# Kernel optimization log

Hardware: AMD Instinct MI355X
Metric: run time of the kernel (lower is better)

The kernel has to match this reference:

```python
import jax, jax.numpy as jnp
import numpy as np

VOCAB = 32000
D_MODEL = 1024
HIDDEN = 2 * D_MODEL
NUM_EXPERTS = 8
TOP_K = 2
B, S = 2, 1024
LN_EPS = 1e-5


def setup_inputs() -> dict:
    key = jax.random.key(0)
    ks = jax.random.split(key, 12)
    sc = 0.02
    return {
        "x": jax.random.randint(ks[0], (B, S), 0, VOCAB),
        "embed": jax.random.normal(ks[1], (VOCAB, D_MODEL), jnp.float32) * sc,
        "Wg": jax.random.normal(ks[2], (D_MODEL, NUM_EXPERTS), jnp.float32) * sc,
        "bg": jnp.zeros((NUM_EXPERTS,), jnp.float32),
        "W1": jax.random.normal(ks[3], (NUM_EXPERTS, D_MODEL, HIDDEN), jnp.float32) * sc,
        "b1": jnp.zeros((NUM_EXPERTS, HIDDEN), jnp.float32),
        "W2": jax.random.normal(ks[4], (NUM_EXPERTS, HIDDEN, D_MODEL), jnp.float32) * sc,
        "b2": jnp.zeros((NUM_EXPERTS, D_MODEL), jnp.float32),
        "gamma": jnp.ones((D_MODEL,), jnp.float32),
        "beta": jnp.zeros((D_MODEL,), jnp.float32),
        "Wh": jax.random.normal(ks[5], (D_MODEL, VOCAB), jnp.float32) * sc,
        "bh": jnp.zeros((VOCAB,), jnp.float32),
    }


def reference(x, embed, Wg, bg, W1, b1, W2, b2, gamma, beta, Wh, bh):
    # forward_pre: embed + gate softmax + top-k
    h = embed[x]                                     # [B,S,d]
    probs = jax.nn.softmax(h @ Wg + bg, axis=-1)     # [B,S,E]
    topk_vals, topk_idx = jax.lax.top_k(probs, TOP_K)  # [B,S,K]
    # combine weights scattered back to dense expert axis: [B,S,E]
    w = jnp.sum(jax.nn.one_hot(topk_idx, NUM_EXPERTS, dtype=h.dtype)
                * topk_vals[..., None], axis=-2)
    # per-expert FFN run densely, masked-combined by gate weights
    a = jax.nn.relu(jnp.einsum('bsd,edh->bseh', h, W1) + b1)   # [B,S,E,H]
    y = jnp.einsum('bseh,ehd->bsed', a, W2) + b2               # [B,S,E,d]
    combined = jnp.einsum('bsed,bse->bsd', y, w)               # [B,S,d]
    # forward_post: LayerNorm + head
    mu = jnp.mean(combined, axis=-1, keepdims=True)
    var = jnp.var(combined, axis=-1, keepdims=True)
    out = (combined - mu) * jax.lax.rsqrt(var + LN_EPS) * gamma + beta
    logits = out @ Wh + bh                                     # [B,S,V]
    return logits.reshape(-1, VOCAB)
```

## Files before the change

kernel.cpp:

```cpp
#include <hip/hip_runtime.h>
#include <hip/hip_bf16.h>
#include <stdint.h>

#define TOKENS 2048
#define DMODEL 1024
#define HID    2048
#define NEXP   8
#define VOCAB  32000
#define ROWCAP 5120
#define MAXTILES 40
#define LN_EPS 1e-5f

typedef __hip_bfloat16 bf16;
typedef __bf16 v8bf __attribute__((ext_vector_type(8)));
typedef float  v4f  __attribute__((ext_vector_type(4)));

#define CTL_COUNTS 0
#define CTL_CURSOR 8
#define CTL_PADOFF 16
#define CTL_TILE2E 32
#define CTL_NTILES 72
#define CTL_INTS   80

typedef __attribute__((address_space(3))) uint32_t lds_u32_t;
typedef __attribute__((address_space(1))) uint32_t glb_u32_t;

__device__ __forceinline__ void gl2lds16(const void* g, void* l) {
  __builtin_amdgcn_global_load_lds((glb_u32_t*)(uintptr_t)g,
                                   (lds_u32_t*)(uintptr_t)l, 16, 0, 0);
}

__global__ __launch_bounds__(256) void embed_gate(
    const int* __restrict__ x, const float* __restrict__ embed,
    const float* __restrict__ Wg, const float* __restrict__ bg,
    bf16* __restrict__ h_bf, int* __restrict__ top2i, float* __restrict__ top2w,
    int* __restrict__ ctl)
{
  const int t = blockIdx.x, tid = threadIdx.x;
  const int xid = x[t];
  const float4 hv = ((const float4*)(embed + (size_t)xid * DMODEL))[tid];

  union { ushort4 u; bf16 b[4]; } pk;
  pk.b[0] = __float2bfloat16(hv.x); pk.b[1] = __float2bfloat16(hv.y);
  pk.b[2] = __float2bfloat16(hv.z); pk.b[3] = __float2bfloat16(hv.w);
  ((ushort4*)(h_bf + (size_t)t * DMODEL))[tid] = pk.u;

  float acc[8] = {0,0,0,0,0,0,0,0};
  const float hk[4] = {hv.x, hv.y, hv.z, hv.w};
  #pragma unroll
  for (int u = 0; u < 4; ++u) {
    const float* wr = Wg + (size_t)(tid*4 + u) * NEXP;
    #pragma unroll
    for (int e = 0; e < 8; ++e) acc[e] += hk[u] * wr[e];
  }
  #pragma unroll
  for (int e = 0; e < 8; ++e)
    for (int off = 32; off >= 1; off >>= 1)
      acc[e] += __shfl_down(acc[e], off, 64);

  __shared__ float sred[4][8];
  const int lane = tid & 63, wave = tid >> 6;
  if (lane == 0) {
    #pragma unroll
    for (int e = 0; e < 8; ++e) sred[wave][e] = acc[e];
  }
  __syncthreads();
  if (tid == 0) {
    float lg[8];
    #pragma unroll
    for (int e = 0; e < 8; ++e)
      lg[e] = sred[0][e] + sred[1][e] + sred[2][e] + sred[3][e] + bg[e];
    float m = lg[0];
    #pragma unroll
    for (int e = 1; e < 8; ++e) m = fmaxf(m, lg[e]);
    float p[8], s = 0.f;
    #pragma unroll
    for (int e = 0; e < 8; ++e) { p[e] = expf(lg[e] - m); s += p[e]; }
    const float inv = 1.f / s;
    int i0 = 0;
    for (int e = 1; e < 8; ++e) if (p[e] > p[i0]) i0 = e;
    int i1 = -1;
    for (int e = 0; e < 8; ++e) { if (e == i0) continue; if (i1 < 0 || p[e] > p[i1]) i1 = e; }
    top2i[2*t] = i0; top2i[2*t+1] = i1;
    top2w[2*t] = p[i0]*inv; top2w[2*t+1] = p[i1]*inv;
    atomicAdd(&ctl[CTL_COUNTS + i0], 1);
    atomicAdd(&ctl[CTL_COUNTS + i1], 1);
  }
}

__global__ __launch_bounds__(256) void scatter_k(
    const int* __restrict__ top2i, int* __restrict__ ctl,
    int* __restrict__ tok2row, int* __restrict__ rowtok)
{
  __shared__ int spad[8];
  const int tid = threadIdx.x;
  for (int r = tid; r < ROWCAP; r += 256) rowtok[r] = 0;
  if (tid == 0) {
    int off = 0, gm = 0;
    for (int e = 0; e < 8; ++e) {
      spad[e] = off; ctl[CTL_PADOFF + e] = off;
      int nt = (ctl[CTL_COUNTS + e] + 127) >> 7;
      for (int i = 0; i < nt; ++i) ctl[CTL_TILE2E + gm++] = e;
      off += nt << 7;
    }
    ctl[CTL_PADOFF + 8] = off;
    ctl[CTL_NTILES] = gm;
  }
  __syncthreads();
  for (int idx = tid; idx < 2*TOKENS; idx += 256) {
    const int e = top2i[idx];
    const int pos = spad[e] + atomicAdd(&ctl[CTL_CURSOR + e], 1);
    tok2row[idx] = pos;
    rowtok[pos] = idx >> 1;
  }
}

__global__ __launch_bounds__(256) void transpose_cvt(
    const float* __restrict__ in, bf16* __restrict__ out, int R, int C)
{
  __shared__ float tile[32][33];
  const int b = blockIdx.z;
  in  += (size_t)b * R * C;
  out += (size_t)b * R * C;
  const int ct = blockIdx.x * 32, rt = blockIdx.y * 32;
  const int lc = threadIdx.x & 31, lr = threadIdx.x >> 5;
  #pragma unroll
  for (int i = 0; i < 4; ++i) {
    const int r = lr + i*8;
    tile[r][lc] = in[(size_t)(rt + r) * C + ct + lc];
  }
  __syncthreads();
  #pragma unroll
  for (int i = 0; i < 4; ++i) {
    const int r = lr + i*8;
    out[(size_t)(ct + r) * R + rt + lc] = __float2bfloat16(tile[lc][r]);
  }
}

template<int MODE>
__global__ __launch_bounds__(256) void gemm128(
    const bf16* __restrict__ Abase, const bf16* __restrict__ Btbase,
    const float* __restrict__ bias, float* __restrict__ outF, bf16* __restrict__ outB,
    const int* __restrict__ ctl, const int* __restrict__ rowtok)
{
  constexpr int K = (MODE == 1) ? HID : DMODEL;
  constexpr int N = (MODE == 0) ? HID : ((MODE == 1) ? DMODEL : VOCAB);
  const int gm = blockIdx.x, gn = blockIdx.y;

  int eid = 0;
  if constexpr (MODE == 0 || MODE == 1) {
    if (gm >= ctl[CTL_NTILES]) return;
    eid = ctl[CTL_TILE2E + gm];
  }

  __shared__ bf16 As[128 * 32];
  __shared__ bf16 Bs[128 * 32];
  __shared__ int  rts[128];

  const int tid = threadIdx.x, lane = tid & 63, wave = tid >> 6;
  const bf16* Bt = Btbase + (size_t)eid * (size_t)N * K + (size_t)(gn * 128) * K;
  const float* bv = bias + (size_t)eid * N + gn * 128;

  if constexpr (MODE == 0) {
    if (tid < 128) rts[tid] = rowtok[gm * 128 + tid];
    __syncthreads();
  }

  const int srow = lane >> 2;
  const int scol = (lane & 3) * 8;
  const int r0 = wave * 16 + srow, r1 = (wave + 4) * 16 + srow;
  size_t ga0, ga1;
  if constexpr (MODE == 0) { ga0 = (size_t)rts[r0]; ga1 = (size_t)rts[r1]; }
  else { ga0 = (size_t)(gm * 128 + r0); ga1 = (size_t)(gm * 128 + r1); }
  const bf16* aptr0 = Abase + ga0 * K + scol;
  const bf16* aptr1 = Abase + ga1 * K + scol;
  const bf16* bptr0 = Bt + (size_t)r0 * K + scol;
  const bf16* bptr1 = Bt + (size_t)r1 * K + scol;

  const int wm = (wave & 1) * 64, wn = (wave >> 1) * 64;
  const int lr = lane & 15, lq = lane >> 4;

  v4f acc[4][4] = {};

  for (int k0 = 0; k0 < K; k0 += 32) {
    gl2lds16(aptr0 + k0, &As[wave * 512]);
    gl2lds16(aptr1 + k0, &As[(wave + 4) * 512]);
    gl2lds16(bptr0 + k0, &Bs[wave * 512]);
    gl2lds16(bptr1 + k0, &Bs[(wave + 4) * 512]);
    __syncthreads();

    v8bf af[4], bfg[4];
    #pragma unroll
    for (int i = 0; i < 4; ++i) af[i]  = *(const v8bf*)&As[(wm + i*16 + lr) * 32 + lq * 8];
    #pragma unroll
    for (int j = 0; j < 4; ++j) bfg[j] = *(const v8bf*)&Bs[(wn + j*16 + lr) * 32 + lq * 8];
    #pragma unroll
    for (int i = 0; i < 4; ++i)
      #pragma unroll
      for (int j = 0; j < 4; ++j)
        acc[i][j] = __builtin_amdgcn_mfma_f32_16x16x32_bf16(af[i], bfg[j], acc[i][j], 0, 0, 0);
    __syncthreads();
  }

  float bb[4];
  #pragma unroll
  for (int j = 0; j < 4; ++j) bb[j] = bv[wn + j*16 + lr];

  #pragma unroll
  for (int i = 0; i < 4; ++i) {
    #pragma unroll
    for (int j = 0; j < 4; ++j) {
      #pragma unroll
      for (int r = 0; r < 4; ++r) {
        const int row = gm * 128 + wm + i*16 + lq*4 + r;
        const int col = gn * 128 + wn + j*16 + lr;
        float v = acc[i][j][r] + bb[j];
        if constexpr (MODE == 0) {
          v = v > 0.f ? v : 0.f;
          outB[(size_t)row * N + col] = __float2bfloat16(v);
        } else {
          outF[(size_t)row * (size_t)N + col] = v;
        }
      }
    }
  }
}

__global__ __launch_bounds__(256) void combine_ln(
    const float* __restrict__ y, const int* __restrict__ tok2row,
    const float* __restrict__ top2w, const float* __restrict__ gamma,
    const float* __restrict__ beta, bf16* __restrict__ ln)
{
  const int t = blockIdx.x, tid = threadIdx.x;
  const int rr0 = tok2row[2*t], rr1 = tok2row[2*t+1];
  const float w0 = top2w[2*t], w1 = top2w[2*t+1];
  const float4 a = ((const float4*)(y + (size_t)rr0 * DMODEL))[tid];
  const float4 b = ((const float4*)(y + (size_t)rr1 * DMODEL))[tid];
  const float c0 = w0*a.x + w1*b.x, c1 = w0*a.y + w1*b.y;
  const float c2 = w0*a.z + w1*b.z, c3 = w0*a.w + w1*b.w;

  float s1 = c0 + c1 + c2 + c3;
  float s2 = c0*c0 + c1*c1 + c2*c2 + c3*c3;
  for (int off = 32; off >= 1; off >>= 1) {
    s1 += __shfl_down(s1, off, 64);
    s2 += __shfl_down(s2, off, 64);
  }
  __shared__ float rs1[4], rs2[4];
  __shared__ float smu, srs;
  const int lane = tid & 63, wave = tid >> 6;
  if (lane == 0) { rs1[wave] = s1; rs2[wave] = s2; }
  __syncthreads();
  if (tid == 0) {
    const float S1 = rs1[0] + rs1[1] + rs1[2] + rs1[3];
    const float S2 = rs2[0] + rs2[1] + rs2[2] + rs2[3];
    const float mu = S1 / DMODEL;
    const float var = S2 / DMODEL - mu * mu;
    smu = mu; srs = rsqrtf(var + LN_EPS);
  }
  __syncthreads();
  const float mu = smu, rstd = srs;
  const float4 g  = ((const float4*)gamma)[tid];
  const float4 be = ((const float4*)beta)[tid];
  union { ushort4 u; bf16 bb[4]; } pk;
  pk.bb[0] = __float2bfloat16((c0 - mu) * rstd * g.x + be.x);
  pk.bb[1] = __float2bfloat16((c1 - mu) * rstd * g.y + be.y);
  pk.bb[2] = __float2bfloat16((c2 - mu) * rstd * g.z + be.z);
  pk.bb[3] = __float2bfloat16((c3 - mu) * rstd * g.w + be.w);
  ((ushort4*)(ln + (size_t)t * DMODEL))[tid] = pk.u;
}

extern "C" void kernel_launch(void* const* d_in, const int* in_sizes, int n_in,
                              void* d_out, int out_size, void* d_ws, size_t ws_size,
                              hipStream_t stream)
{
  (void)in_sizes; (void)n_in; (void)out_size; (void)ws_size;
  const int*   x     = (const int*)d_in[0];
  const float* embed = (const float*)d_in[1];
  const float* Wg    = (const float*)d_in[2];
  const float* bg    = (const float*)d_in[3];
  const float* W1    = (const float*)d_in[4];
  const float* b1    = (const float*)d_in[5];
  const float* W2    = (const float*)d_in[6];
  const float* b2    = (const float*)d_in[7];
  const float* gamma = (const float*)d_in[8];
  const float* beta  = (const float*)d_in[9];
  const float* Wh    = (const float*)d_in[10];
  const float* bh    = (const float*)d_in[11];
  float* out = (float*)d_out;

  char* ws = (char*)d_ws;
  size_t o = 0;
  int* ctl = (int*)(ws + o);        o += 1024;
  bf16* h_bf = (bf16*)(ws + o);     o += (size_t)TOKENS * DMODEL * 2;
  int* top2i = (int*)(ws + o);      o += (size_t)TOKENS * 2 * 4;
  float* top2w = (float*)(ws + o);  o += (size_t)TOKENS * 2 * 4;
  int* tok2row = (int*)(ws + o);    o += (size_t)TOKENS * 2 * 4;
  int* rowtok = (int*)(ws + o);     o += (size_t)ROWCAP * 4;
  o = (o + 255) & ~(size_t)255;
  bf16* a_act = (bf16*)(ws + o);    o += (size_t)ROWCAP * HID * 2;
  float* yrow = (float*)(ws + o);   o += (size_t)ROWCAP * DMODEL * 4;
  bf16* lnb = (bf16*)(ws + o);      o += (size_t)TOKENS * DMODEL * 2;
  bf16* W1t = (bf16*)(ws + o);      o += (size_t)NEXP * DMODEL * HID * 2;
  bf16* W2t = (bf16*)(ws + o);      o += (size_t)NEXP * DMODEL * HID * 2;
  bf16* Wht = (bf16*)(ws + o);      o += (size_t)DMODEL * VOCAB * 2;

  hipMemsetAsync(ctl, 0, CTL_INTS * sizeof(int), stream);
  embed_gate<<<TOKENS, 256, 0, stream>>>(x, embed, Wg, bg, h_bf, top2i, top2w, ctl);
  scatter_k<<<1, 256, 0, stream>>>(top2i, ctl, tok2row, rowtok);
  transpose_cvt<<<dim3(HID/32, DMODEL/32, NEXP), 256, 0, stream>>>(W1, W1t, DMODEL, HID);
  transpose_cvt<<<dim3(DMODEL/32, HID/32, NEXP), 256, 0, stream>>>(W2, W2t, HID, DMODEL);
  transpose_cvt<<<dim3(VOCAB/32, DMODEL/32, 1), 256, 0, stream>>>(Wh, Wht, DMODEL, VOCAB);
  gemm128<0><<<dim3(MAXTILES, HID/128), 256, 0, stream>>>(h_bf, W1t, b1, nullptr, a_act, ctl, rowtok);
  gemm128<1><<<dim3(MAXTILES, DMODEL/128), 256, 0, stream>>>(a_act, W2t, b2, yrow, nullptr, ctl, nullptr);
  combine_ln<<<TOKENS, 256, 0, stream>>>(yrow, tok2row, top2w, gamma, beta, lnb);
  gemm128<2><<<dim3(TOKENS/128, VOCAB/128), 256, 0, stream>>>(lnb, Wht, bh, out, nullptr, nullptr, nullptr);
}
```

Baseline: 866.8 us.

## Replace head GEMM with 256x256-tile, 512-thread double-buffered MFMA kernel

Replaces the vocab-projection GEMM, previously a 128x128-tile kernel, with a dedicated 256x256-tile kernel. It uses 8 waves, 128KB of dynamic LDS with double buffering via direct global-to-LDS loads, interleaved stage/compute phases with priority hints and sched barriers, and a remapped block order for L2 locality. The head GEMM dominates runtime, and larger tiles cut global and LDS traffic per FLOP while overlapping loads with MFMA work. The risks are lower occupancy from the large LDS footprint and correctness that depends on hand-counted vmcnt waits.

```diff
diff --git a/kernel.cpp b/kernel.cpp
--- a/kernel.cpp
+++ b/kernel.cpp
@@ -144,14 +144,12 @@
     const int* __restrict__ ctl, const int* __restrict__ rowtok)
 {
   constexpr int K = (MODE == 1) ? HID : DMODEL;
-  constexpr int N = (MODE == 0) ? HID : ((MODE == 1) ? DMODEL : VOCAB);
+  constexpr int N = (MODE == 0) ? HID : DMODEL;
   const int gm = blockIdx.x, gn = blockIdx.y;
 
   int eid = 0;
-  if constexpr (MODE == 0 || MODE == 1) {
-    if (gm >= ctl[CTL_NTILES]) return;
-    eid = ctl[CTL_TILE2E + gm];
-  }
+  if (gm >= ctl[CTL_NTILES]) return;
+  eid = ctl[CTL_TILE2E + gm];
 
   __shared__ bf16 As[128 * 32];
   __shared__ bf16 Bs[128 * 32];
@@ -224,6 +222,161 @@
       }
     }
   }
+}
+
+
+__device__ __forceinline__ void stageAB(const bf16* g, char* l) {
+  gl2lds16(g,      l);
+  gl2lds16(g + 32, l + 8192);
+}
+
+#define SBAR() do { __builtin_amdgcn_sched_barrier(0); \
+                    __builtin_amdgcn_s_barrier();       \
+                    __builtin_amdgcn_sched_barrier(0); } while (0)
+
+__global__ __launch_bounds__(512, 2) void gemm256(
+    const bf16* __restrict__ A, const bf16* __restrict__ Bt,
+    const float* __restrict__ bias, float* __restrict__ out)
+{
+  extern __shared__ char smem[];
+  constexpr int K = DMODEL;
+  constexpr int N = VOCAB;
+  constexpr int NK = K / 64;
+
+  const int orig = blockIdx.y * 8 + blockIdx.x;
+  const int p = (orig & 7) * 125 + (orig >> 3);
+  const int tm0 = (p & 7) * 256;
+  const int tn0 = (p >> 3) * 256;
+
+  const int tid = threadIdx.x;
+  const int lane = tid & 63, wv = tid >> 6;
+  const int lr = lane & 15, lq = lane >> 4;
+  const int wr = wv >> 2, wc = wv & 3;
+
+  const int r_s = tid >> 2;
+  const int c_s = (tid & 3) * 8;
+  const bf16* aG = A  + (size_t)(tm0 + r_s) * K + c_s;
+  const bf16* bG = Bt + (size_t)(tn0 + r_s) * K + c_s;
+  char* lW = smem + wv * 1024;
+
+  const int aOff = wr * 16384 + lr * 64 + lq * 16;
+  const int bOff = 32768 + (wc >> 1) * 16384 + ((wc & 1) * 64 + lr) * 64 + lq * 16;
+
+  v4f acc[8][4] = {};
+  v8bf Af[4][2], Bf[4][2];
+
+  stageAB(aG,          lW);
+  stageAB(aG + 131072, lW + 16384);
+  stageAB(bG,          lW + 32768);
+  stageAB(bG + 131072, lW + 32768 + 16384);
+  stageAB(aG + 64,           lW + 65536);
+  stageAB(aG + 131072 + 64,  lW + 65536 + 16384);
+  stageAB(bG + 64,           lW + 65536 + 32768);
+  stageAB(bG + 131072 + 64,  lW + 65536 + 32768 + 16384);
+  asm volatile("s_waitcnt vmcnt(8)" ::: "memory");
+  __builtin_amdgcn_s_barrier();
+  __builtin_amdgcn_sched_barrier(0);
+
+  for (int kt = 0; kt < NK; ++kt) {
+    const int db = kt & 1;
+    const char* sA = smem + db * 65536 + aOff;
+    const char* sB = smem + db * 65536 + bOff;
+    char* lwA = lW + (db ^ 1) * 65536;
+    char* lwB = lW + db * 65536 + 32768;
+    const int kN1 = (kt + 1) * 64;
+    const int kN2 = (kt + 2) * 64;
+    const bool stA = (kt > 0) & (kt + 1 < NK);
+    const bool stB = (kt + 2 < NK);
+
+    #pragma unroll
+    for (int mi = 0; mi < 4; ++mi)
+      #pragma unroll
+      for (int kk = 0; kk < 2; ++kk)
+        Af[mi][kk] = *(const v8bf*)(sA + kk * 8192 + mi * 1024);
+    #pragma unroll
+    for (int n = 0; n < 2; ++n)
+      #pragma unroll
+      for (int kk = 0; kk < 2; ++kk)
+        Bf[n][kk] = *(const v8bf*)(sB + kk * 8192 + n * 1024);
+    if (stA) stageAB(aG + kN1, lwA);
+    SBAR();
+    __builtin_amdgcn_s_setprio(1);
+    #pragma unroll
+    for (int mi = 0; mi < 4; ++mi)
+      #pragma unroll
+      for (int n = 0; n < 2; ++n) {
+        acc[mi][n] = __builtin_amdgcn_mfma_f32_16x16x32_bf16(Af[mi][0], Bf[n][0], acc[mi][n], 0, 0, 0);
+        acc[mi][n] = __builtin_amdgcn_mfma_f32_16x16x32_bf16(Af[mi][1], Bf[n][1], acc[mi][n], 0, 0, 0);
+      }
+    __builtin_amdgcn_s_setprio(0);
+    SBAR();
+
+    #pragma unroll
+    for (int n = 2; n < 4; ++n)
+      #pragma unroll
+      for (int kk = 0; kk < 2; ++kk)
+        Bf[n][kk] = *(const v8bf*)(sB + kk * 8192 + n * 1024);
+    if (stA) stageAB(aG + 131072 + kN1, lwA + 16384);
+    SBAR();
+    __builtin_amdgcn_s_setprio(1);
+    #pragma unroll
+    for (int mi = 0; mi < 4; ++mi)
+      #pragma unroll
+      for (int n = 2; n < 4; ++n) {
+        acc[mi][n] = __builtin_amdgcn_mfma_f32_16x16x32_bf16(Af[mi][0], Bf[n][0], acc[mi][n], 0, 0, 0);
+        acc[mi][n] = __builtin_amdgcn_mfma_f32_16x16x32_bf16(Af[mi][1], Bf[n][1], acc[mi][n], 0, 0, 0);
+      }
+    __builtin_amdgcn_s_setprio(0);
+    SBAR();
+
+    #pragma unroll
+    for (int mi = 0; mi < 4; ++mi)
+      #pragma unroll
+      for (int kk = 0; kk < 2; ++kk)
+        Af[mi][kk] = *(const v8bf*)(sA + kk * 8192 + (4 + mi) * 1024);
+    if (stB) stageAB(bG + kN2, lwB);
+    SBAR();
+    __builtin_amdgcn_s_setprio(1);
+    #pragma unroll
+    for (int mi = 0; mi < 4; ++mi)
+      #pragma unroll
+      for (int n = 2; n < 4; ++n) {
+        acc[4 + mi][n] = __builtin_amdgcn_mfma_f32_16x16x32_bf16(Af[mi][0], Bf[n][0], acc[4 + mi][n], 0, 0, 0);
+        acc[4 + mi][n] = __builtin_amdgcn_mfma_f32_16x16x32_bf16(Af[mi][1], Bf[n][1], acc[4 + mi][n], 0, 0, 0);
+      }
+    __builtin_amdgcn_s_setprio(0);
+    SBAR();
+
+    if (stB) stageAB(bG + 131072 + kN2, lwB + 16384);
+    SBAR();
+    __builtin_amdgcn_s_setprio(1);
+    #pragma unroll
+    for (int mi = 0; mi < 4; ++mi)
+      #pragma unroll
+      for (int n = 0; n < 2; ++n) {
+        acc[4 + mi][n] = __builtin_amdgcn_mfma_f32_16x16x32_bf16(Af[mi][0], Bf[n][0], acc[4 + mi][n], 0, 0, 0);
+        acc[4 + mi][n] = __builtin_amdgcn_mfma_f32_16x16x32_bf16(Af[mi][1], Bf[n][1], acc[4 + mi][n], 0, 0, 0);
+      }
+    __builtin_amdgcn_s_setprio(0);
+    __builtin_amdgcn_sched_barrier(0);
+    if (stB) { asm volatile("s_waitcnt vmcnt(4)" ::: "memory"); }
+    else     { asm volatile("s_waitcnt vmcnt(0)" ::: "memory"); }
+    __builtin_amdgcn_s_barrier();
+    __builtin_amdgcn_sched_barrier(0);
+  }
+
+  const int col0 = tn0 + wc * 64 + lr;
+  const size_t row0 = (size_t)(tm0 + wr * 128 + lq * 4);
+  float bb[4];
+  #pragma unroll
+  for (int n = 0; n < 4; ++n) bb[n] = bias[col0 + n * 16];
+  #pragma unroll
+  for (int mi = 0; mi < 8; ++mi)
+    #pragma unroll
+    for (int n = 0; n < 4; ++n)
+      #pragma unroll
+      for (int rr = 0; rr < 4; ++rr)
+        out[(row0 + mi * 16 + rr) * (size_t)N + col0 + n * 16] = acc[mi][n][rr] + bb[n];
 }
 
 __global__ __launch_bounds__(256) void combine_ln(
@@ -313,5 +466,8 @@
   gemm128<0><<<dim3(MAXTILES, HID/128), 256, 0, stream>>>(h_bf, W1t, b1, nullptr, a_act, ctl, rowtok);
   gemm128<1><<<dim3(MAXTILES, DMODEL/128), 256, 0, stream>>>(a_act, W2t, b2, yrow, nullptr, ctl, nullptr);
   combine_ln<<<TOKENS, 256, 0, stream>>>(yrow, tok2row, top2w, gamma, beta, lnb);
-  gemm128<2><<<dim3(TOKENS/128, VOCAB/128), 256, 0, stream>>>(lnb, Wht, bh, out, nullptr, nullptr, nullptr);
-}
+
+  hipFuncSetAttribute(reinterpret_cast<const void*>(gemm256),
+                      hipFuncAttributeMaxDynamicSharedMemorySize, 131072);
+  gemm256<<<dim3(8, VOCAB/256), 512, 131072, stream>>>(lnb, Wht, bh, out);
+}
```

Result: faster. 847.5 us (-2.2%).

## Add double-buffered 256x128 head GEMM and XOR-swizzle LDS in expert GEMMs

Applied to the files above, without the earlier changes.

Replaces the vocab head projection with a dedicated 512-thread kernel. It uses 256x128 tiles, double-buffered LDS prefetch of the next K slice during MFMA work, and s_setprio around the MFMA block. Both this kernel and the expert GEMMs now XOR-swizzle LDS columns to reduce bank conflicts on fragment reads. The head kernel assumes tile counts divide exactly, uses 48KB of shared memory, and block ordering groups 8 M-tiles per N-tile for reuse of the weight slice.

```diff
diff --git a/kernel.cpp b/kernel.cpp
--- a/kernel.cpp
+++ b/kernel.cpp
@@ -144,14 +144,12 @@
     const int* __restrict__ ctl, const int* __restrict__ rowtok)
 {
   constexpr int K = (MODE == 1) ? HID : DMODEL;
-  constexpr int N = (MODE == 0) ? HID : ((MODE == 1) ? DMODEL : VOCAB);
+  constexpr int N = (MODE == 0) ? HID : DMODEL;
   const int gm = blockIdx.x, gn = blockIdx.y;
 
   int eid = 0;
-  if constexpr (MODE == 0 || MODE == 1) {
-    if (gm >= ctl[CTL_NTILES]) return;
-    eid = ctl[CTL_TILE2E + gm];
-  }
+  if (gm >= ctl[CTL_NTILES]) return;
+  eid = ctl[CTL_TILE2E + gm];
 
   __shared__ bf16 As[128 * 32];
   __shared__ bf16 Bs[128 * 32];
@@ -167,7 +165,7 @@
   }
 
   const int srow = lane >> 2;
-  const int scol = (lane & 3) * 8;
+  const int scol = 8 * ((lane & 3) ^ ((lane >> 2) & 3));
   const int r0 = wave * 16 + srow, r1 = (wave + 4) * 16 + srow;
   size_t ga0, ga1;
   if constexpr (MODE == 0) { ga0 = (size_t)rts[r0]; ga1 = (size_t)rts[r1]; }
@@ -179,6 +177,7 @@
 
   const int wm = (wave & 1) * 64, wn = (wave >> 1) * 64;
   const int lr = lane & 15, lq = lane >> 4;
+  const int rot = (lq ^ (lr & 3)) * 8;
 
   v4f acc[4][4] = {};
 
@@ -191,9 +190,9 @@
 
     v8bf af[4], bfg[4];
     #pragma unroll
-    for (int i = 0; i < 4; ++i) af[i]  = *(const v8bf*)&As[(wm + i*16 + lr) * 32 + lq * 8];
-    #pragma unroll
-    for (int j = 0; j < 4; ++j) bfg[j] = *(const v8bf*)&Bs[(wn + j*16 + lr) * 32 + lq * 8];
+    for (int i = 0; i < 4; ++i) af[i]  = *(const v8bf*)&As[(wm + i*16 + lr) * 32 + rot];
+    #pragma unroll
+    for (int j = 0; j < 4; ++j) bfg[j] = *(const v8bf*)&Bs[(wn + j*16 + lr) * 32 + rot];
     #pragma unroll
     for (int i = 0; i < 4; ++i)
       #pragma unroll
@@ -224,6 +223,88 @@
       }
     }
   }
+}
+
+__global__ __launch_bounds__(512, 4) void gemm_head(
+    const bf16* __restrict__ A, const bf16* __restrict__ Bt,
+    const float* __restrict__ bias, float* __restrict__ out)
+{
+  constexpr int K = DMODEL;
+  constexpr int N = VOCAB;
+  __shared__ char smem[49152];
+
+  const int orig = blockIdx.x;
+  const int tm0 = (orig & 7) * 256;
+  const int tn0 = (orig >> 3) * 128;
+
+  const int tid = threadIdx.x;
+  const int lane = tid & 63, wv = tid >> 6;
+  const int lr = lane & 15, lq = lane >> 4;
+  const int wr = wv & 3, wc = wv >> 2;
+
+  const int r_s = tid >> 2;
+  const int c_s = 8 * ((tid & 3) ^ ((tid >> 2) & 3));
+  const bf16* aP0 = A  + (size_t)(tm0 + r_s) * K + c_s;
+  const bf16* aP1 = A  + (size_t)(tm0 + 128 + r_s) * K + c_s;
+  const bf16* bP  = Bt + (size_t)(tn0 + r_s) * K + c_s;
+  char* const dA0 = smem + wv * 1024;
+  char* const dA1 = smem + 8192 + wv * 1024;
+  char* const dB  = smem + 32768 + wv * 1024;
+
+  const int rot = (lq ^ (lr & 3)) * 16;
+  const int aRd = (wr * 64 + lr) * 64 + rot;
+  const int bRd = 32768 + (wc * 64 + lr) * 64 + rot;
+
+  v4f acc[4][4] = {};
+
+  gl2lds16(aP0, dA0);
+  gl2lds16(aP1, dA1);
+  gl2lds16(bP,  dB);
+  asm volatile("s_waitcnt vmcnt(0)" ::: "memory");
+  __builtin_amdgcn_s_barrier();
+  __builtin_amdgcn_sched_barrier(0);
+
+  for (int kt = 0; kt < 32; ++kt) {
+    const int cur = kt & 1;
+    if (kt < 31) {
+      const int k0n = (kt + 1) * 32;
+      const int nb = cur ^ 1;
+      gl2lds16(aP0 + k0n, dA0 + nb * 16384);
+      gl2lds16(aP1 + k0n, dA1 + nb * 16384);
+      gl2lds16(bP  + k0n, dB  + nb * 8192);
+    }
+    const char* sa = smem + cur * 16384 + aRd;
+    const char* sb = smem + cur * 8192  + bRd;
+    v8bf a[4], b[4];
+    #pragma unroll
+    for (int i = 0; i < 4; ++i) a[i] = *(const v8bf*)(sa + i * 1024);
+    #pragma unroll
+    for (int j = 0; j < 4; ++j) b[j] = *(const v8bf*)(sb + j * 1024);
+    __builtin_amdgcn_s_setprio(1);
+    #pragma unroll
+    for (int i = 0; i < 4; ++i)
+      #pragma unroll
+      for (int j = 0; j < 4; ++j)
+        acc[i][j] = __builtin_amdgcn_mfma_f32_16x16x32_bf16(a[i], b[j], acc[i][j], 0, 0, 0);
+    __builtin_amdgcn_s_setprio(0);
+    __builtin_amdgcn_sched_barrier(0);
+    asm volatile("s_waitcnt vmcnt(0)" ::: "memory");
+    __builtin_amdgcn_s_barrier();
+    __builtin_amdgcn_sched_barrier(0);
+  }
+
+  const int col0 = tn0 + wc * 64 + lr;
+  const size_t row0 = (size_t)(tm0 + wr * 64 + lq * 4);
+  float bb[4];
+  #pragma unroll
+  for (int j = 0; j < 4; ++j) bb[j] = bias[col0 + j * 16];
+  #pragma unroll
+  for (int i = 0; i < 4; ++i)
+    #pragma unroll
+    for (int j = 0; j < 4; ++j)
+      #pragma unroll
+      for (int r = 0; r < 4; ++r)
+        out[(row0 + i * 16 + r) * (size_t)N + col0 + j * 16] = acc[i][j][r] + bb[j];
 }
 
 __global__ __launch_bounds__(256) void combine_ln(
@@ -313,5 +394,6 @@
   gemm128<0><<<dim3(MAXTILES, HID/128), 256, 0, stream>>>(h_bf, W1t, b1, nullptr, a_act, ctl, rowtok);
   gemm128<1><<<dim3(MAXTILES, DMODEL/128), 256, 0, stream>>>(a_act, W2t, b2, yrow, nullptr, ctl, nullptr);
   combine_ln<<<TOKENS, 256, 0, stream>>>(yrow, tok2row, top2w, gamma, beta, lnb);
-  gemm128<2><<<dim3(TOKENS/128, VOCAB/128), 256, 0, stream>>>(lnb, Wht, bh, out, nullptr, nullptr, nullptr);
-}
+
+  gemm_head<<<dim3(2000), 512, 0, stream>>>(lnb, Wht, bh, out);
+}
```

Result: faster. 836.4 us (-3.5%).
